# Kernel optimization log

Measured on AMD Instinct MI355X. Metric: run time of the kernel, lower is better.

## Reference

```python
import jax, jax.numpy as jnp
import numpy as np
import math


def setup_inputs() -> dict:
    key = jax.random.key(0)
    k1, k2, k3 = jax.random.split(key, 3)
    B, L, H, E = 2, 2048, 8, 64
    queries = jax.random.normal(k1, (B, L, H, E), dtype=jnp.float32)
    keys = jax.random.normal(k2, (B, L, H, E), dtype=jnp.float32)
    values = jax.random.normal(k3, (B, L, H, E), dtype=jnp.float32)
    return {"queries": queries, "keys": keys, "values": values}


def reference(queries, keys, values):
    B, L, H, E = queries.shape
    scale = 1.0 / math.sqrt(E)
    # [B,H,L,S] attention scores
    scores = jnp.einsum('blhe,bshe->bhls', queries, keys)
    # causal mask: positions s > l masked to -inf (scale * -inf stays -inf)
    causal = jnp.triu(jnp.ones((L, L), dtype=bool), k=1)  # True above diagonal
    scores = jnp.where(causal[None, None, :, :], -jnp.inf, scores)
    attn = scale * scores
    SA = jax.nn.softmax(attn, axis=-1)  # dropout p=0.0 -> identity
    V = jnp.einsum('bhls,bshd->blhd', SA, values)
    return (V, SA)
```

## Files before the change

### kernel.cpp

```cpp
#include <hip/hip_runtime.h>
#include <math.h>

#define L_DIM 2048
#define H_DIM 8
#define E_DIM 64
#define ROWSTRIDE (H_DIM * E_DIM)
#define NT 256
#define LDP 72

typedef __attribute__((ext_vector_type(8))) short short8;
typedef __attribute__((ext_vector_type(4))) float floatx4;

__device__ __forceinline__ unsigned short f2bf(float f) {
    unsigned int u = __builtin_bit_cast(unsigned int, f);
    u += 0x7fffu + ((u >> 16) & 1u);
    return (unsigned short)(u >> 16);
}

__global__ __launch_bounds__(NT)
void attn_mfma_kernel(const float* __restrict__ Q,
                      const float* __restrict__ K,
                      const float* __restrict__ Vv,
                      float* __restrict__ outV,
                      float* __restrict__ outSA)
{
    __shared__ __align__(16) unsigned short Qs[64][LDP];
    __shared__ __align__(16) unsigned short Ks[64][LDP];
    __shared__ __align__(16) unsigned short Vt[64][LDP];
    __shared__ __align__(16) unsigned short Ps[64][LDP];

    const int t   = threadIdx.x;
    const int bid = blockIdx.x;
    const int idx = bid & 31;
    const int qt  = (idx & 1) ? (31 - (idx >> 1)) : (idx >> 1);
    const int bh  = bid >> 5;
    const int h   = bh & 7;
    const int b   = bh >> 3;
    const int q0  = qt << 6;

    const int lane = t & 63;
    const int w    = t >> 6;
    const int l15  = lane & 15;
    const int quad = lane >> 4;

    const float* Qbase = Q  + ((size_t)b * L_DIM * ROWSTRIDE) + (size_t)h * E_DIM;
    const float* Kbase = K  + ((size_t)b * L_DIM * ROWSTRIDE) + (size_t)h * E_DIM;
    const float* Vbase = Vv + ((size_t)b * L_DIM * ROWSTRIDE) + (size_t)h * E_DIM;
    float* saBase = outSA + ((size_t)(b * H_DIM + h)) * L_DIM * L_DIM;

    const int sr = t >> 2;
    const int se = (t & 3) * 16;

    {
        const float* src = Qbase + (size_t)(q0 + sr) * ROWSTRIDE + se;
        float4 f0 = *(const float4*)(src + 0);
        float4 f1 = *(const float4*)(src + 4);
        float4 f2 = *(const float4*)(src + 8);
        float4 f3 = *(const float4*)(src + 12);
        union { unsigned short u[8]; short8 v; } p0, p1;
        p0.u[0]=f2bf(f0.x*0.125f); p0.u[1]=f2bf(f0.y*0.125f); p0.u[2]=f2bf(f0.z*0.125f); p0.u[3]=f2bf(f0.w*0.125f);
        p0.u[4]=f2bf(f1.x*0.125f); p0.u[5]=f2bf(f1.y*0.125f); p0.u[6]=f2bf(f1.z*0.125f); p0.u[7]=f2bf(f1.w*0.125f);
        p1.u[0]=f2bf(f2.x*0.125f); p1.u[1]=f2bf(f2.y*0.125f); p1.u[2]=f2bf(f2.z*0.125f); p1.u[3]=f2bf(f2.w*0.125f);
        p1.u[4]=f2bf(f3.x*0.125f); p1.u[5]=f2bf(f3.y*0.125f); p1.u[6]=f2bf(f3.z*0.125f); p1.u[7]=f2bf(f3.w*0.125f);
        *(short8*)&Qs[sr][se]     = p0.v;
        *(short8*)&Qs[sr][se + 8] = p1.v;
    }
    __syncthreads();

    const short8 aQ0 = *(const short8*)&Qs[16 * w + l15][quad * 8];
    const short8 aQ1 = *(const short8*)&Qs[16 * w + l15][32 + quad * 8];

    float m_r[4], l_r[4];
#pragma unroll
    for (int r = 0; r < 4; ++r) { m_r[r] = -INFINITY; l_r[r] = 0.0f; }

    const int ntiles = qt + 1;

    for (int st = 0; st < ntiles; ++st) {
        const int s0 = st << 6;
        __syncthreads();
        {
            const float* src = Kbase + (size_t)(s0 + sr) * ROWSTRIDE + se;
            float4 f0 = *(const float4*)(src + 0);
            float4 f1 = *(const float4*)(src + 4);
            float4 f2 = *(const float4*)(src + 8);
            float4 f3 = *(const float4*)(src + 12);
            union { unsigned short u[8]; short8 v; } p0, p1;
            p0.u[0]=f2bf(f0.x); p0.u[1]=f2bf(f0.y); p0.u[2]=f2bf(f0.z); p0.u[3]=f2bf(f0.w);
            p0.u[4]=f2bf(f1.x); p0.u[5]=f2bf(f1.y); p0.u[6]=f2bf(f1.z); p0.u[7]=f2bf(f1.w);
            p1.u[0]=f2bf(f2.x); p1.u[1]=f2bf(f2.y); p1.u[2]=f2bf(f2.z); p1.u[3]=f2bf(f2.w);
            p1.u[4]=f2bf(f3.x); p1.u[5]=f2bf(f3.y); p1.u[6]=f2bf(f3.z); p1.u[7]=f2bf(f3.w);
            *(short8*)&Ks[sr][se]     = p0.v;
            *(short8*)&Ks[sr][se + 8] = p1.v;
        }
        __syncthreads();

        floatx4 d[4];
#pragma unroll
        for (int j = 0; j < 4; ++j) {
            short8 b0 = *(const short8*)&Ks[16 * j + l15][quad * 8];
            short8 b1 = *(const short8*)&Ks[16 * j + l15][32 + quad * 8];
            floatx4 acc = {0.f, 0.f, 0.f, 0.f};
            acc = __builtin_amdgcn_mfma_f32_16x16x32_bf16(aQ0, b0, acc, 0, 0, 0);
            acc = __builtin_amdgcn_mfma_f32_16x16x32_bf16(aQ1, b1, acc, 0, 0, 0);
            d[j] = acc;
        }

        const bool diag = (st == qt);
#pragma unroll
        for (int r = 0; r < 4; ++r) {
            const int lrow = q0 + 16 * w + quad * 4 + r;
            float v0 = d[0][r], v1 = d[1][r], v2 = d[2][r], v3 = d[3][r];
            if (diag) {
                v0 = (s0 +  0 + l15 <= lrow) ? v0 : -INFINITY;
                v1 = (s0 + 16 + l15 <= lrow) ? v1 : -INFINITY;
                v2 = (s0 + 32 + l15 <= lrow) ? v2 : -INFINITY;
                v3 = (s0 + 48 + l15 <= lrow) ? v3 : -INFINITY;
            }
            float vm = fmaxf(fmaxf(v0, v1), fmaxf(v2, v3));
#pragma unroll
            for (int mk = 1; mk < 16; mk <<= 1) vm = fmaxf(vm, __shfl_xor(vm, mk));
            const float mnew = fmaxf(m_r[r], vm);
            float es = __expf(v0 - mnew) + __expf(v1 - mnew) +
                       __expf(v2 - mnew) + __expf(v3 - mnew);
#pragma unroll
            for (int mk = 1; mk < 16; mk <<= 1) es += __shfl_xor(es, mk);
            l_r[r] = l_r[r] * __expf(m_r[r] - mnew) + es;
            m_r[r] = mnew;
        }
    }

    float invl[4];
#pragma unroll
    for (int r = 0; r < 4; ++r) invl[r] = 1.0f / l_r[r];

    floatx4 oacc[4];
#pragma unroll
    for (int j = 0; j < 4; ++j) oacc[j] = (floatx4){0.f, 0.f, 0.f, 0.f};

    for (int st = 0; st < ntiles; ++st) {
        const int s0 = st << 6;
        __syncthreads();
        {
            const float* src = Kbase + (size_t)(s0 + sr) * ROWSTRIDE + se;
            float4 f0 = *(const float4*)(src + 0);
            float4 f1 = *(const float4*)(src + 4);
            float4 f2 = *(const float4*)(src + 8);
            float4 f3 = *(const float4*)(src + 12);
            union { unsigned short u[8]; short8 v; } p0, p1;
            p0.u[0]=f2bf(f0.x); p0.u[1]=f2bf(f0.y); p0.u[2]=f2bf(f0.z); p0.u[3]=f2bf(f0.w);
            p0.u[4]=f2bf(f1.x); p0.u[5]=f2bf(f1.y); p0.u[6]=f2bf(f1.z); p0.u[7]=f2bf(f1.w);
            p1.u[0]=f2bf(f2.x); p1.u[1]=f2bf(f2.y); p1.u[2]=f2bf(f2.z); p1.u[3]=f2bf(f2.w);
            p1.u[4]=f2bf(f3.x); p1.u[5]=f2bf(f3.y); p1.u[6]=f2bf(f3.z); p1.u[7]=f2bf(f3.w);
            *(short8*)&Ks[sr][se]     = p0.v;
            *(short8*)&Ks[sr][se + 8] = p1.v;
        }
        {
            const float* src = Vbase + (size_t)(s0 + sr) * ROWSTRIDE + se;
            float4 f0 = *(const float4*)(src + 0);
            float4 f1 = *(const float4*)(src + 4);
            float4 f2 = *(const float4*)(src + 8);
            float4 f3 = *(const float4*)(src + 12);
            Vt[se +  0][sr] = f2bf(f0.x); Vt[se +  1][sr] = f2bf(f0.y);
            Vt[se +  2][sr] = f2bf(f0.z); Vt[se +  3][sr] = f2bf(f0.w);
            Vt[se +  4][sr] = f2bf(f1.x); Vt[se +  5][sr] = f2bf(f1.y);
            Vt[se +  6][sr] = f2bf(f1.z); Vt[se +  7][sr] = f2bf(f1.w);
            Vt[se +  8][sr] = f2bf(f2.x); Vt[se +  9][sr] = f2bf(f2.y);
            Vt[se + 10][sr] = f2bf(f2.z); Vt[se + 11][sr] = f2bf(f2.w);
            Vt[se + 12][sr] = f2bf(f3.x); Vt[se + 13][sr] = f2bf(f3.y);
            Vt[se + 14][sr] = f2bf(f3.z); Vt[se + 15][sr] = f2bf(f3.w);
        }
        __syncthreads();

        floatx4 d[4];
#pragma unroll
        for (int j = 0; j < 4; ++j) {
            short8 b0 = *(const short8*)&Ks[16 * j + l15][quad * 8];
            short8 b1 = *(const short8*)&Ks[16 * j + l15][32 + quad * 8];
            floatx4 acc = {0.f, 0.f, 0.f, 0.f};
            acc = __builtin_amdgcn_mfma_f32_16x16x32_bf16(aQ0, b0, acc, 0, 0, 0);
            acc = __builtin_amdgcn_mfma_f32_16x16x32_bf16(aQ1, b1, acc, 0, 0, 0);
            d[j] = acc;
        }

        const bool diag = (st == qt);
#pragma unroll
        for (int r = 0; r < 4; ++r) {
            const int lrow = q0 + 16 * w + quad * 4 + r;
            float* sap = saBase + (size_t)lrow * L_DIM + s0 + l15;
            const float mr = m_r[r], il = invl[r];
#pragma unroll
            for (int j = 0; j < 4; ++j) {
                float v = d[j][r];
                bool ok = !diag || (s0 + 16 * j + l15 <= lrow);
                float p = ok ? __expf(v - mr) * il : 0.0f;
                sap[16 * j] = p;
                Ps[16 * w + quad * 4 + r][16 * j + l15] = f2bf(p);
            }
        }

        short8 aP0 = *(const short8*)&Ps[16 * w + l15][quad * 8];
        short8 aP1 = *(const short8*)&Ps[16 * w + l15][32 + quad * 8];
#pragma unroll
        for (int j = 0; j < 4; ++j) {
            short8 bv0 = *(const short8*)&Vt[16 * j + l15][quad * 8];
            short8 bv1 = *(const short8*)&Vt[16 * j + l15][32 + quad * 8];
            oacc[j] = __builtin_amdgcn_mfma_f32_16x16x32_bf16(aP0, bv0, oacc[j], 0, 0, 0);
            oacc[j] = __builtin_amdgcn_mfma_f32_16x16x32_bf16(aP1, bv1, oacc[j], 0, 0, 0);
        }
    }

#pragma unroll
    for (int r = 0; r < 4; ++r) {
        const int lrow = q0 + 16 * w + quad * 4 + r;
        float* op = outV + ((size_t)b * L_DIM + lrow) * ROWSTRIDE + (size_t)h * E_DIM + l15;
#pragma unroll
        for (int j = 0; j < 4; ++j) op[16 * j] = oacc[j][r];
    }

    {
        const int z0 = (qt + 1) << 6;
        float* rowp = saBase + (size_t)(q0 + sr) * L_DIM;
        const float4 zf = {0.f, 0.f, 0.f, 0.f};
        for (int s = z0 + (t & 3) * 4; s < L_DIM; s += 16)
            *(float4*)(rowp + s) = zf;
    }
}

extern "C" void kernel_launch(void* const* d_in, const int* in_sizes, int n_in,
                              void* d_out, int out_size, void* d_ws, size_t ws_size,
                              hipStream_t stream) {
    const float* Q  = (const float*)d_in[0];
    const float* K  = (const float*)d_in[1];
    const float* Vv = (const float*)d_in[2];
    float* out   = (float*)d_out;
    float* outV  = out;
    float* outSA = out + (size_t)2 * L_DIM * H_DIM * E_DIM;

    dim3 grid(2 * H_DIM * 32);
    dim3 block(NT);
    attn_mfma_kernel<<<grid, block, 0, stream>>>(Q, K, Vv, outV, outSA);
}
```

Baseline: 400.2 us.

## Split key tiles across two warp groups per block and merge softmax stats

Doubles the block to 512 threads, with two 256-thread groups processing alternating key tiles for the same query tile. Each group keeps its own K/V/P shared buffers, and the per-row max and sum are merged through shared memory before the second pass. Partial outputs are combined through a shared buffer at the end. It also folds log2(e) into the Q scale so it can use exp2, and simplifies bf16 rounding to round-half-up. This raises parallelism per block, at the cost of more shared memory (about 64KB), extra syncs, and idle groups on odd tile counts.

```diff
diff --git a/kernel.cpp b/kernel.cpp
--- a/kernel.cpp
+++ b/kernel.cpp
@@ -3,33 +3,43 @@
 
 #define L_DIM 2048
 #define H_DIM 8
-#define E_DIM 64
-#define ROWSTRIDE (H_DIM * E_DIM)
-#define NT 256
-#define LDP 72
+#define ROWSTRIDE 512
+#define NT 512
+#define QSCALE 0.18033688011112042f
 
 typedef __attribute__((ext_vector_type(8))) short short8;
 typedef __attribute__((ext_vector_type(4))) float floatx4;
 
 __device__ __forceinline__ unsigned short f2bf(float f) {
     unsigned int u = __builtin_bit_cast(unsigned int, f);
-    u += 0x7fffu + ((u >> 16) & 1u);
-    return (unsigned short)(u >> 16);
-}
-
-__global__ __launch_bounds__(NT)
-void attn_mfma_kernel(const float* __restrict__ Q,
-                      const float* __restrict__ K,
-                      const float* __restrict__ Vv,
-                      float* __restrict__ outV,
-                      float* __restrict__ outSA)
+    return (unsigned short)((u + 0x8000u) >> 16);
+}
+
+__device__ __forceinline__ float fexp2(float x) {
+#if __has_builtin(__builtin_amdgcn_exp2f)
+    return __builtin_amdgcn_exp2f(x);
+#else
+    return exp2f(x);
+#endif
+}
+
+__global__ __launch_bounds__(NT, 4)
+void attn_mfma2(const float* __restrict__ Q, const float* __restrict__ K,
+                const float* __restrict__ Vv, float* __restrict__ outV,
+                float* __restrict__ outSA)
 {
-    __shared__ __align__(16) unsigned short Qs[64][LDP];
-    __shared__ __align__(16) unsigned short Ks[64][LDP];
-    __shared__ __align__(16) unsigned short Vt[64][LDP];
-    __shared__ __align__(16) unsigned short Ps[64][LDP];
+    __shared__ __align__(16) unsigned char smem[65536];
+    unsigned short* Qs = (unsigned short*)(smem);
+    unsigned short* Ks = (unsigned short*)(smem + 9216);
+    unsigned short* Vt = (unsigned short*)(smem + 27648);
+    unsigned short* Ps = (unsigned short*)(smem + 46080);
+    float* Ml = (float*)(smem + 64512);
+    float* Ll = (float*)(smem + 65024);
+    float* Ob = (float*)(smem + 9216);
 
     const int t   = threadIdx.x;
+    const int g   = t >> 8;
+    const int u   = t & 255;
     const int bid = blockIdx.x;
     const int idx = bid & 31;
     const int qt  = (idx & 1) ? (31 - (idx >> 1)) : (idx >> 1);
@@ -39,77 +49,79 @@
     const int q0  = qt << 6;
 
     const int lane = t & 63;
-    const int w    = t >> 6;
+    const int wg   = (t >> 6) & 3;
     const int l15  = lane & 15;
     const int quad = lane >> 4;
 
-    const float* Qbase = Q  + ((size_t)b * L_DIM * ROWSTRIDE) + (size_t)h * E_DIM;
-    const float* Kbase = K  + ((size_t)b * L_DIM * ROWSTRIDE) + (size_t)h * E_DIM;
-    const float* Vbase = Vv + ((size_t)b * L_DIM * ROWSTRIDE) + (size_t)h * E_DIM;
-    float* saBase = outSA + ((size_t)(b * H_DIM + h)) * L_DIM * L_DIM;
-
-    const int sr = t >> 2;
-    const int se = (t & 3) * 16;
+    const float* Qb = Q  + (size_t)b * L_DIM * ROWSTRIDE + h * 64;
+    const float* Kb = K  + (size_t)b * L_DIM * ROWSTRIDE + h * 64;
+    const float* Vb = Vv + (size_t)b * L_DIM * ROWSTRIDE + h * 64;
+    float* saBase = outSA + (size_t)(b * H_DIM + h) * L_DIM * L_DIM;
 
     {
-        const float* src = Qbase + (size_t)(q0 + sr) * ROWSTRIDE + se;
-        float4 f0 = *(const float4*)(src + 0);
+        const int sr = t >> 3, se = (t & 7) * 8;
+        const float* src = Qb + (size_t)(q0 + sr) * ROWSTRIDE + se;
+        float4 f0 = *(const float4*)(src);
         float4 f1 = *(const float4*)(src + 4);
-        float4 f2 = *(const float4*)(src + 8);
-        float4 f3 = *(const float4*)(src + 12);
-        union { unsigned short u[8]; short8 v; } p0, p1;
-        p0.u[0]=f2bf(f0.x*0.125f); p0.u[1]=f2bf(f0.y*0.125f); p0.u[2]=f2bf(f0.z*0.125f); p0.u[3]=f2bf(f0.w*0.125f);
-        p0.u[4]=f2bf(f1.x*0.125f); p0.u[5]=f2bf(f1.y*0.125f); p0.u[6]=f2bf(f1.z*0.125f); p0.u[7]=f2bf(f1.w*0.125f);
-        p1.u[0]=f2bf(f2.x*0.125f); p1.u[1]=f2bf(f2.y*0.125f); p1.u[2]=f2bf(f2.z*0.125f); p1.u[3]=f2bf(f2.w*0.125f);
-        p1.u[4]=f2bf(f3.x*0.125f); p1.u[5]=f2bf(f3.y*0.125f); p1.u[6]=f2bf(f3.z*0.125f); p1.u[7]=f2bf(f3.w*0.125f);
-        *(short8*)&Qs[sr][se]     = p0.v;
-        *(short8*)&Qs[sr][se + 8] = p1.v;
-    }
-    __syncthreads();
-
-    const short8 aQ0 = *(const short8*)&Qs[16 * w + l15][quad * 8];
-    const short8 aQ1 = *(const short8*)&Qs[16 * w + l15][32 + quad * 8];
+        union { unsigned short us[8]; short8 v; } p;
+        p.us[0] = f2bf(f0.x * QSCALE); p.us[1] = f2bf(f0.y * QSCALE);
+        p.us[2] = f2bf(f0.z * QSCALE); p.us[3] = f2bf(f0.w * QSCALE);
+        p.us[4] = f2bf(f1.x * QSCALE); p.us[5] = f2bf(f1.y * QSCALE);
+        p.us[6] = f2bf(f1.z * QSCALE); p.us[7] = f2bf(f1.w * QSCALE);
+        *(short8*)&Qs[sr * 72 + se] = p.v;
+    }
+    __syncthreads();
+
+    const short8 aQ0 = *(const short8*)&Qs[(16 * wg + l15) * 72 + quad * 8];
+    const short8 aQ1 = *(const short8*)&Qs[(16 * wg + l15) * 72 + 32 + quad * 8];
+
+    const int ntiles = qt + 1;
+    const int niter  = (ntiles + 1) >> 1;
+    const int ksr = u >> 2, kse = (u & 3) * 16;
+    unsigned short* myKs = Ks + g * 4608;
+    unsigned short* myVt = Vt + g * 4608;
+    unsigned short* myPs = Ps + g * 4608;
 
     float m_r[4], l_r[4];
 #pragma unroll
-    for (int r = 0; r < 4; ++r) { m_r[r] = -INFINITY; l_r[r] = 0.0f; }
-
-    const int ntiles = qt + 1;
-
-    for (int st = 0; st < ntiles; ++st) {
+    for (int r = 0; r < 4; ++r) { m_r[r] = -INFINITY; l_r[r] = 0.f; }
+
+    for (int it = 0; it < niter; ++it) {
+        const int st = 2 * it + g;
+        const bool active = (st < ntiles);
         const int s0 = st << 6;
         __syncthreads();
-        {
-            const float* src = Kbase + (size_t)(s0 + sr) * ROWSTRIDE + se;
+        if (active) {
+            const float* src = Kb + (size_t)(s0 + ksr) * ROWSTRIDE + kse;
             float4 f0 = *(const float4*)(src + 0);
             float4 f1 = *(const float4*)(src + 4);
             float4 f2 = *(const float4*)(src + 8);
             float4 f3 = *(const float4*)(src + 12);
-            union { unsigned short u[8]; short8 v; } p0, p1;
-            p0.u[0]=f2bf(f0.x); p0.u[1]=f2bf(f0.y); p0.u[2]=f2bf(f0.z); p0.u[3]=f2bf(f0.w);
-            p0.u[4]=f2bf(f1.x); p0.u[5]=f2bf(f1.y); p0.u[6]=f2bf(f1.z); p0.u[7]=f2bf(f1.w);
-            p1.u[0]=f2bf(f2.x); p1.u[1]=f2bf(f2.y); p1.u[2]=f2bf(f2.z); p1.u[3]=f2bf(f2.w);
-            p1.u[4]=f2bf(f3.x); p1.u[5]=f2bf(f3.y); p1.u[6]=f2bf(f3.z); p1.u[7]=f2bf(f3.w);
-            *(short8*)&Ks[sr][se]     = p0.v;
-            *(short8*)&Ks[sr][se + 8] = p1.v;
-        }
-        __syncthreads();
+            union { unsigned short us[8]; short8 v; } p0, p1;
+            p0.us[0]=f2bf(f0.x); p0.us[1]=f2bf(f0.y); p0.us[2]=f2bf(f0.z); p0.us[3]=f2bf(f0.w);
+            p0.us[4]=f2bf(f1.x); p0.us[5]=f2bf(f1.y); p0.us[6]=f2bf(f1.z); p0.us[7]=f2bf(f1.w);
+            p1.us[0]=f2bf(f2.x); p1.us[1]=f2bf(f2.y); p1.us[2]=f2bf(f2.z); p1.us[3]=f2bf(f2.w);
+            p1.us[4]=f2bf(f3.x); p1.us[5]=f2bf(f3.y); p1.us[6]=f2bf(f3.z); p1.us[7]=f2bf(f3.w);
+            *(short8*)&myKs[ksr * 72 + kse]     = p0.v;
+            *(short8*)&myKs[ksr * 72 + kse + 8] = p1.v;
+        }
+        __syncthreads();
+        if (!active) continue;
 
         floatx4 d[4];
 #pragma unroll
         for (int j = 0; j < 4; ++j) {
-            short8 b0 = *(const short8*)&Ks[16 * j + l15][quad * 8];
-            short8 b1 = *(const short8*)&Ks[16 * j + l15][32 + quad * 8];
+            short8 b0 = *(const short8*)&myKs[(16 * j + l15) * 72 + quad * 8];
+            short8 b1 = *(const short8*)&myKs[(16 * j + l15) * 72 + 32 + quad * 8];
             floatx4 acc = {0.f, 0.f, 0.f, 0.f};
             acc = __builtin_amdgcn_mfma_f32_16x16x32_bf16(aQ0, b0, acc, 0, 0, 0);
             acc = __builtin_amdgcn_mfma_f32_16x16x32_bf16(aQ1, b1, acc, 0, 0, 0);
             d[j] = acc;
         }
-
         const bool diag = (st == qt);
 #pragma unroll
         for (int r = 0; r < 4; ++r) {
-            const int lrow = q0 + 16 * w + quad * 4 + r;
+            const int lrow = q0 + 16 * wg + quad * 4 + r;
             float v0 = d[0][r], v1 = d[1][r], v2 = d[2][r], v3 = d[3][r];
             if (diag) {
                 v0 = (s0 +  0 + l15 <= lrow) ? v0 : -INFINITY;
@@ -121,108 +133,152 @@
 #pragma unroll
             for (int mk = 1; mk < 16; mk <<= 1) vm = fmaxf(vm, __shfl_xor(vm, mk));
             const float mnew = fmaxf(m_r[r], vm);
-            float es = __expf(v0 - mnew) + __expf(v1 - mnew) +
-                       __expf(v2 - mnew) + __expf(v3 - mnew);
+            float es = fexp2(v0 - mnew) + fexp2(v1 - mnew) +
+                       fexp2(v2 - mnew) + fexp2(v3 - mnew);
 #pragma unroll
             for (int mk = 1; mk < 16; mk <<= 1) es += __shfl_xor(es, mk);
-            l_r[r] = l_r[r] * __expf(m_r[r] - mnew) + es;
+            l_r[r] = l_r[r] * fexp2(m_r[r] - mnew) + es;
             m_r[r] = mnew;
         }
     }
 
-    float invl[4];
-#pragma unroll
-    for (int r = 0; r < 4; ++r) invl[r] = 1.0f / l_r[r];
+    __syncthreads();
+    if (l15 == 0) {
+#pragma unroll
+        for (int r = 0; r < 4; ++r) {
+            const int row = 16 * wg + quad * 4 + r;
+            Ml[g * 64 + row] = m_r[r];
+            Ll[g * 64 + row] = l_r[r];
+        }
+    }
+    __syncthreads();
+    float mfin[4], invl[4];
+#pragma unroll
+    for (int r = 0; r < 4; ++r) {
+        const int row = 16 * wg + quad * 4 + r;
+        float m0 = Ml[row], m1 = Ml[64 + row];
+        float l0 = Ll[row], l1 = Ll[64 + row];
+        float mf = fmaxf(m0, m1);
+        float lf = l0 * fexp2(m0 - mf) + l1 * fexp2(m1 - mf);
+        mfin[r] = mf;
+        invl[r] = 1.0f / lf;
+    }
 
     floatx4 oacc[4];
 #pragma unroll
     for (int j = 0; j < 4; ++j) oacc[j] = (floatx4){0.f, 0.f, 0.f, 0.f};
 
-    for (int st = 0; st < ntiles; ++st) {
+    for (int it = 0; it < niter; ++it) {
+        const int st = 2 * it + g;
+        const bool active = (st < ntiles);
         const int s0 = st << 6;
         __syncthreads();
-        {
-            const float* src = Kbase + (size_t)(s0 + sr) * ROWSTRIDE + se;
-            float4 f0 = *(const float4*)(src + 0);
-            float4 f1 = *(const float4*)(src + 4);
-            float4 f2 = *(const float4*)(src + 8);
-            float4 f3 = *(const float4*)(src + 12);
-            union { unsigned short u[8]; short8 v; } p0, p1;
-            p0.u[0]=f2bf(f0.x); p0.u[1]=f2bf(f0.y); p0.u[2]=f2bf(f0.z); p0.u[3]=f2bf(f0.w);
-            p0.u[4]=f2bf(f1.x); p0.u[5]=f2bf(f1.y); p0.u[6]=f2bf(f1.z); p0.u[7]=f2bf(f1.w);
-            p1.u[0]=f2bf(f2.x); p1.u[1]=f2bf(f2.y); p1.u[2]=f2bf(f2.z); p1.u[3]=f2bf(f2.w);
-            p1.u[4]=f2bf(f3.x); p1.u[5]=f2bf(f3.y); p1.u[6]=f2bf(f3.z); p1.u[7]=f2bf(f3.w);
-            *(short8*)&Ks[sr][se]     = p0.v;
-            *(short8*)&Ks[sr][se + 8] = p1.v;
-        }
-        {
-            const float* src = Vbase + (size_t)(s0 + sr) * ROWSTRIDE + se;
-            float4 f0 = *(const float4*)(src + 0);
-            float4 f1 = *(const float4*)(src + 4);
-            float4 f2 = *(const float4*)(src + 8);
-            float4 f3 = *(const float4*)(src + 12);
-            Vt[se +  0][sr] = f2bf(f0.x); Vt[se +  1][sr] = f2bf(f0.y);
-            Vt[se +  2][sr] = f2bf(f0.z); Vt[se +  3][sr] = f2bf(f0.w);
-            Vt[se +  4][sr] = f2bf(f1.x); Vt[se +  5][sr] = f2bf(f1.y);
-            Vt[se +  6][sr] = f2bf(f1.z); Vt[se +  7][sr] = f2bf(f1.w);
-            Vt[se +  8][sr] = f2bf(f2.x); Vt[se +  9][sr] = f2bf(f2.y);
-            Vt[se + 10][sr] = f2bf(f2.z); Vt[se + 11][sr] = f2bf(f2.w);
-            Vt[se + 12][sr] = f2bf(f3.x); Vt[se + 13][sr] = f2bf(f3.y);
-            Vt[se + 14][sr] = f2bf(f3.z); Vt[se + 15][sr] = f2bf(f3.w);
-        }
-        __syncthreads();
+        if (active) {
+            {
+                const float* src = Kb + (size_t)(s0 + ksr) * ROWSTRIDE + kse;
+                float4 f0 = *(const float4*)(src + 0);
+                float4 f1 = *(const float4*)(src + 4);
+                float4 f2 = *(const float4*)(src + 8);
+                float4 f3 = *(const float4*)(src + 12);
+                union { unsigned short us[8]; short8 v; } p0, p1;
+                p0.us[0]=f2bf(f0.x); p0.us[1]=f2bf(f0.y); p0.us[2]=f2bf(f0.z); p0.us[3]=f2bf(f0.w);
+                p0.us[4]=f2bf(f1.x); p0.us[5]=f2bf(f1.y); p0.us[6]=f2bf(f1.z); p0.us[7]=f2bf(f1.w);
+                p1.us[0]=f2bf(f2.x); p1.us[1]=f2bf(f2.y); p1.us[2]=f2bf(f2.z); p1.us[3]=f2bf(f2.w);
+                p1.us[4]=f2bf(f3.x); p1.us[5]=f2bf(f3.y); p1.us[6]=f2bf(f3.z); p1.us[7]=f2bf(f3.w);
+                *(short8*)&myKs[ksr * 72 + kse]     = p0.v;
+                *(short8*)&myKs[ksr * 72 + kse + 8] = p1.v;
+            }
+            {
+                const float* src = Vb + (size_t)(s0 + ksr) * ROWSTRIDE + kse;
+                float4 f0 = *(const float4*)(src + 0);
+                float4 f1 = *(const float4*)(src + 4);
+                float4 f2 = *(const float4*)(src + 8);
+                float4 f3 = *(const float4*)(src + 12);
+                myVt[(kse +  0) * 72 + ksr] = f2bf(f0.x);
+                myVt[(kse +  1) * 72 + ksr] = f2bf(f0.y);
+                myVt[(kse +  2) * 72 + ksr] = f2bf(f0.z);
+                myVt[(kse +  3) * 72 + ksr] = f2bf(f0.w);
+                myVt[(kse +  4) * 72 + ksr] = f2bf(f1.x);
+                myVt[(kse +  5) * 72 + ksr] = f2bf(f1.y);
+                myVt[(kse +  6) * 72 + ksr] = f2bf(f1.z);
+                myVt[(kse +  7) * 72 + ksr] = f2bf(f1.w);
+                myVt[(kse +  8) * 72 + ksr] = f2bf(f2.x);
+                myVt[(kse +  9) * 72 + ksr] = f2bf(f2.y);
+                myVt[(kse + 10) * 72 + ksr] = f2bf(f2.z);
+                myVt[(kse + 11) * 72 + ksr] = f2bf(f2.w);
+                myVt[(kse + 12) * 72 + ksr] = f2bf(f3.x);
+                myVt[(kse + 13) * 72 + ksr] = f2bf(f3.y);
+                myVt[(kse + 14) * 72 + ksr] = f2bf(f3.z);
+                myVt[(kse + 15) * 72 + ksr] = f2bf(f3.w);
+            }
+        }
+        __syncthreads();
+        if (!active) continue;
 
         floatx4 d[4];
 #pragma unroll
         for (int j = 0; j < 4; ++j) {
-            short8 b0 = *(const short8*)&Ks[16 * j + l15][quad * 8];
-            short8 b1 = *(const short8*)&Ks[16 * j + l15][32 + quad * 8];
+            short8 b0 = *(const short8*)&myKs[(16 * j + l15) * 72 + quad * 8];
+            short8 b1 = *(const short8*)&myKs[(16 * j + l15) * 72 + 32 + quad * 8];
             floatx4 acc = {0.f, 0.f, 0.f, 0.f};
             acc = __builtin_amdgcn_mfma_f32_16x16x32_bf16(aQ0, b0, acc, 0, 0, 0);
             acc = __builtin_amdgcn_mfma_f32_16x16x32_bf16(aQ1, b1, acc, 0, 0, 0);
             d[j] = acc;
         }
-
         const bool diag = (st == qt);
 #pragma unroll
         for (int r = 0; r < 4; ++r) {
-            const int lrow = q0 + 16 * w + quad * 4 + r;
+            const int lrow = q0 + 16 * wg + quad * 4 + r;
             float* sap = saBase + (size_t)lrow * L_DIM + s0 + l15;
-            const float mr = m_r[r], il = invl[r];
+            const float mr = mfin[r], il = invl[r];
 #pragma unroll
             for (int j = 0; j < 4; ++j) {
                 float v = d[j][r];
                 bool ok = !diag || (s0 + 16 * j + l15 <= lrow);
-                float p = ok ? __expf(v - mr) * il : 0.0f;
+                float p = ok ? fexp2(v - mr) * il : 0.0f;
                 sap[16 * j] = p;
-                Ps[16 * w + quad * 4 + r][16 * j + l15] = f2bf(p);
-            }
-        }
-
-        short8 aP0 = *(const short8*)&Ps[16 * w + l15][quad * 8];
-        short8 aP1 = *(const short8*)&Ps[16 * w + l15][32 + quad * 8];
+                myPs[(16 * wg + quad * 4 + r) * 72 + 16 * j + l15] = f2bf(p);
+            }
+        }
+        short8 aP0 = *(const short8*)&myPs[(16 * wg + l15) * 72 + quad * 8];
+        short8 aP1 = *(const short8*)&myPs[(16 * wg + l15) * 72 + 32 + quad * 8];
 #pragma unroll
         for (int j = 0; j < 4; ++j) {
-            short8 bv0 = *(const short8*)&Vt[16 * j + l15][quad * 8];
-            short8 bv1 = *(const short8*)&Vt[16 * j + l15][32 + quad * 8];
+            short8 bv0 = *(const short8*)&myVt[(16 * j + l15) * 72 + quad * 8];
+            short8 bv1 = *(const short8*)&myVt[(16 * j + l15) * 72 + 32 + quad * 8];
             oacc[j] = __builtin_amdgcn_mfma_f32_16x16x32_bf16(aP0, bv0, oacc[j], 0, 0, 0);
             oacc[j] = __builtin_amdgcn_mfma_f32_16x16x32_bf16(aP1, bv1, oacc[j], 0, 0, 0);
         }
     }
 
-#pragma unroll
-    for (int r = 0; r < 4; ++r) {
-        const int lrow = q0 + 16 * w + quad * 4 + r;
-        float* op = outV + ((size_t)b * L_DIM + lrow) * ROWSTRIDE + (size_t)h * E_DIM + l15;
-#pragma unroll
-        for (int j = 0; j < 4; ++j) op[16 * j] = oacc[j][r];
+    __syncthreads();
+    if (g == 1) {
+#pragma unroll
+        for (int r = 0; r < 4; ++r) {
+            const int row = 16 * wg + quad * 4 + r;
+#pragma unroll
+            for (int j = 0; j < 4; ++j)
+                Ob[row * 65 + 16 * j + l15] = oacc[j][r];
+        }
+    }
+    __syncthreads();
+    if (g == 0) {
+#pragma unroll
+        for (int r = 0; r < 4; ++r) {
+            const int row = 16 * wg + quad * 4 + r;
+            float* op = outV + ((size_t)b * L_DIM + q0 + row) * ROWSTRIDE + h * 64 + l15;
+#pragma unroll
+            for (int j = 0; j < 4; ++j)
+                op[16 * j] = oacc[j][r] + Ob[row * 65 + 16 * j + l15];
+        }
     }
 
     {
-        const int z0 = (qt + 1) << 6;
-        float* rowp = saBase + (size_t)(q0 + sr) * L_DIM;
+        const int z0 = ntiles << 6;
+        const int zr = t >> 3;
+        float* rowp = saBase + (size_t)(q0 + zr) * L_DIM;
         const float4 zf = {0.f, 0.f, 0.f, 0.f};
-        for (int s = z0 + (t & 3) * 4; s < L_DIM; s += 16)
+        for (int s = z0 + (t & 7) * 4; s < L_DIM; s += 32)
             *(float4*)(rowp + s) = zf;
     }
 }
@@ -235,9 +291,9 @@
     const float* Vv = (const float*)d_in[2];
     float* out   = (float*)d_out;
     float* outV  = out;
-    float* outSA = out + (size_t)2 * L_DIM * H_DIM * E_DIM;
+    float* outSA = out + (size_t)2 * L_DIM * H_DIM * 64;
 
     dim3 grid(2 * H_DIM * 32);
     dim3 block(NT);
-    attn_mfma_kernel<<<grid, block, 0, stream>>>(Q, K, Vv, outV, outSA);
-}
+    attn_mfma2<<<grid, block, 0, stream>>>(Q, K, Vv, outV, outSA);
+}
```

After: 389.9 us. 1.03x faster.
